# Kernel tuning notes

Measured on AMD Instinct MI355X. Metric: run time of the kernel, lower is better.

The kernel has to match this reference:

```python
import jax, jax.numpy as jnp
import numpy as np

WINDOW_SIZE = 11
CHANNEL = 3
PAD = WINDOW_SIZE // 2
C1 = 0.01 ** 2
C2 = 0.03 ** 2
LEVEL_WEIGHTS = np.array([0.0448, 0.2856, 0.3001, 0.2363, 0.1333], dtype=np.float32)


def _make_window():
    # 1D Gaussian, sigma=1.5, normalized; outer product -> 2D window
    x = np.arange(WINDOW_SIZE, dtype=np.float32)
    g = np.exp(-((x - WINDOW_SIZE // 2) ** 2) / (2.0 * 1.5 ** 2))
    g = g / g.sum()
    w2 = np.outer(g, g).astype(np.float32)  # [11,11]
    # depthwise kernel [C, 1, 11, 11]
    return jnp.asarray(np.tile(w2[None, None], (CHANNEL, 1, 1, 1)))


def setup_inputs() -> dict:
    key = jax.random.key(0)
    k1, k2 = jax.random.split(key)
    img1 = jax.random.uniform(k1, (16, 3, 512, 512), dtype=jnp.float32)
    # correlated second image so cs stays positive (cs**weight well-defined)
    img2 = jnp.clip(img1 + 0.05 * jax.random.normal(k2, img1.shape, dtype=jnp.float32), 0.0, 1.0)
    return {"img1": img1, "img2": img2, "window": _make_window()}


def _dwconv(x, window):
    # depthwise 11x11 conv, SAME padding (pad=5), groups=C
    return jax.lax.conv_general_dilated(
        x, window, window_strides=(1, 1), padding=[(PAD, PAD), (PAD, PAD)],
        feature_group_count=CHANNEL,
        dimension_numbers=("NCHW", "OIHW", "NCHW"))


def _ssim_and_cs(img1, img2, window):
    mu1 = _dwconv(img1, window)
    mu2 = _dwconv(img2, window)
    mu1_sq = mu1 * mu1
    mu2_sq = mu2 * mu2
    mu1_mu2 = mu1 * mu2
    sigma1_sq = _dwconv(img1 * img1, window) - mu1_sq
    sigma2_sq = _dwconv(img2 * img2, window) - mu2_sq
    sigma12 = _dwconv(img1 * img2, window) - mu1_mu2
    cs_map = (2.0 * sigma12 + C2) / (sigma1_sq + sigma2_sq + C2)
    ssim_map = (2.0 * mu1_mu2 + C1) / (mu1_sq + mu2_sq + C1) * cs_map
    return jnp.mean(ssim_map), jnp.mean(cs_map)


def _avg_pool2(x):
    B, C, H, W = x.shape
    return x.reshape(B, C, H // 2, 2, W // 2, 2).mean(axis=(3, 5))


def reference(img1, img2, window):
    weights = jnp.asarray(LEVEL_WEIGHTS)
    levels = weights.shape[0]
    mssim, mcs = [], []
    for i in range(levels):
        s, c = _ssim_and_cs(img1, img2, window)
        mssim.append(s)
        mcs.append(c)
        if i < levels - 1:
            img1 = _avg_pool2(img1)
            img2 = _avg_pool2(img2)
    mssim = jnp.stack(mssim)
    mcs = jnp.stack(mcs)
    return jnp.prod(mcs[:-1] ** weights[:-1]) * mssim[-1] ** weights[-1]
```

## Files before the change

kernel.cpp:

```cpp
#include <hip/hip_runtime.h>
#include <math.h>

#define TW 16
#define SS 58
#define HS 64
#define SC1 0.0001f
#define SC2 0.0009f
#define PLANES 48
#define NSLOT 64

template<int HRt>
struct alignas(16) SmemT {
    float sb[HRt * SS];
    float hb[HRt * HS];
    float rbuf[8];
};

template<int THt>
__device__ __forceinline__ void ssim_tile(
        SmemT<THt + 10>* sm,
        const float* __restrict__ p1, const float* __restrict__ p2,
        int H, int W, int tx, int ty, int level,
        const float* __restrict__ window,
        float* __restrict__ accum,
        float* __restrict__ l1a, float* __restrict__ l1b,
        float* __restrict__ l2a, float* __restrict__ l2b,
        float* __restrict__ l3a, float* __restrict__ l3b,
        float* __restrict__ l4a, float* __restrict__ l4b)
{
    constexpr int HRt = THt + 10;
    const int tid = threadIdx.x;
    float* sb = sm->sb;
    float* hb = sm->hb;

    float g[11];
    {
        float invg5 = 1.0f / sqrtf(window[60]);
        #pragma unroll
        for (int k = 0; k < 11; ++k) g[k] = window[55 + k] * invg5;
    }

    const bool interior = (ty >= 5) && (ty + HRt - 6 < H) &&
                          (tx >= 6) && (tx + 22 <= W);
    if (interior) {
        for (int s = tid; s < HRt * 14; s += 256) {
            int r = s / 14, j = s - r * 14;
            size_t o = (size_t)(ty + r - 5) * W + (tx - 6 + 2 * j);
            float2 v1 = *(const float2*)(p1 + o);
            float2 v2 = *(const float2*)(p2 + o);
            float* d = &sb[SS * r + 4 * j];
            *(float2*)(d)     = make_float2(v1.x + v2.x, v1.x - v2.x);
            *(float2*)(d + 2) = make_float2(v1.y + v2.y, v1.y - v2.y);
        }
    } else {
        for (int s = tid; s < HRt * 14; s += 256) {
            int r = s / 14, j = s - r * 14;
            int gy = ty + r - 5;
            int gx = tx - 6 + 2 * j;
            float2 v1 = make_float2(0.f, 0.f), v2 = make_float2(0.f, 0.f);
            if ((unsigned)gy < (unsigned)H && (unsigned)gx < (unsigned)W) {
                size_t o = (size_t)gy * W + gx;
                v1 = *(const float2*)(p1 + o);
                v2 = *(const float2*)(p2 + o);
            }
            float* d = &sb[SS * r + 4 * j];
            *(float2*)(d)     = make_float2(v1.x + v2.x, v1.x - v2.x);
            *(float2*)(d + 2) = make_float2(v1.y + v2.y, v1.y - v2.y);
        }
    }
    __syncthreads();

    if (l1a) {
        int pc = tid & 7;
        int pr = tid >> 3;
        int r  = 2 * pr + 5;
        int x0 = 2 * (2 * pc + 6);
        const float* a0 = &sb[SS * r + x0];
        float2 p00 = *(const float2*)(a0);
        float2 p01 = *(const float2*)(a0 + 2);
        float2 p10 = *(const float2*)(a0 + SS);
        float2 p11 = *(const float2*)(a0 + SS + 2);
        float su = p00.x + p01.x + p10.x + p11.x;
        float sv = p00.y + p01.y + p10.y + p11.y;
        int W2 = W >> 1;
        size_t o = (size_t)((ty >> 1) + pr) * W2 + (tx >> 1) + pc;
        l1a[o] = 0.125f * (su + sv);
        l1b[o] = 0.125f * (su - sv);
    }

    if (l1a && tid >= 192) {
        const int lane = tid - 192;
        int qr = lane >> 2, qc = lane & 3;
        int rb = 4 * qr + 5, cb = 4 * qc + 6;
        float su = 0.f, sv = 0.f;
        #pragma unroll
        for (int i = 0; i < 4; ++i) {
            int ii = (i + qc) & 3;
            #pragma unroll
            for (int j = 0; j < 4; ++j) {
                int jr = (j + qr) & 3;
                float2 p = *(const float2*)&sb[SS * (rb + ii) + 2 * (cb + jr)];
                su += p.x; sv += p.y;
            }
        }
        float v2a = 0.03125f * (su + sv), v2b = 0.03125f * (su - sv);
        {
            int W4 = W >> 2;
            size_t o = (size_t)((ty >> 2) + qr) * W4 + (tx >> 2) + qc;
            l2a[o] = v2a;
            l2b[o] = v2b;
        }
        float v3a, v3b;
        {
            int tr = (lane >> 1) & 7, tc = lane & 1;
            int l00 = 8 * tr + 2 * tc;
            v3a = 0.25f * (__shfl(v2a, l00) + __shfl(v2a, l00 + 1) +
                           __shfl(v2a, l00 + 4) + __shfl(v2a, l00 + 5));
            v3b = 0.25f * (__shfl(v2b, l00) + __shfl(v2b, l00 + 1) +
                           __shfl(v2b, l00 + 4) + __shfl(v2b, l00 + 5));
            if (lane < 16) {
                int W8 = W >> 3;
                size_t o = (size_t)((ty >> 3) + tr) * W8 + (tx >> 3) + tc;
                l3a[o] = v3a;
                l3b[o] = v3b;
            }
        }
        {
            int ur = lane & 3;
            float v4a = 0.25f * (__shfl(v3a, 4 * ur) + __shfl(v3a, 4 * ur + 1) +
                                 __shfl(v3a, 4 * ur + 2) + __shfl(v3a, 4 * ur + 3));
            float v4b = 0.25f * (__shfl(v3b, 4 * ur) + __shfl(v3b, 4 * ur + 1) +
                                 __shfl(v3b, 4 * ur + 2) + __shfl(v3b, 4 * ur + 3));
            if (lane < 4) {
                int W16 = W >> 4;
                size_t o = (size_t)((ty >> 4) + ur) * W16 + (tx >> 4);
                l4a[o] = v4a;
                l4b[o] = v4b;
            }
        }
    }

    for (int gi = tid; gi < HRt * 8; gi += 256) {
        int r  = gi >> 3;
        int c0 = (gi & 7) << 1;
        const float* src = &sb[SS * r + 2 * (c0 + 1)];
        float mua = 0, mva = 0, qua = 0, qva = 0;
        float mub = 0, mvb = 0, qub = 0, qvb = 0;
        #pragma unroll
        for (int k = 0; k < 12; ++k) {
            float2 uv = *(const float2*)(src + 2 * k);
            float u = uv.x, v = uv.y;
            float u2 = u * u, v2 = v * v;
            if (k < 11) {
                float gk = g[k];
                mua = fmaf(gk, u,  mua);
                mva = fmaf(gk, v,  mva);
                qua = fmaf(gk, u2, qua);
                qva = fmaf(gk, v2, qva);
            }
            if (k >= 1) {
                float gk = g[k - 1];
                mub = fmaf(gk, u,  mub);
                mvb = fmaf(gk, v,  mvb);
                qub = fmaf(gk, u2, qub);
                qvb = fmaf(gk, v2, qvb);
            }
        }
        int rx = (r & 1) << 2;
        *(float4*)&hb[HS * r + ((4 * c0)     ^ rx)] = make_float4(mua, mva, qua, qva);
        *(float4*)&hb[HS * r + ((4 * c0 + 4) ^ rx)] = make_float4(mub, mvb, qub, qvb);
    }
    __syncthreads();

    float ssum = 0.f, csum = 0.f;
    if (tid < 4 * THt) {
        int c  = tid & 15;
        int r0 = (tid >> 4) << 2;
        float MU[4] = {0, 0, 0, 0}, MV[4] = {0, 0, 0, 0};
        float QU[4] = {0, 0, 0, 0}, QV[4] = {0, 0, 0, 0};
        #pragma unroll
        for (int k = 0; k < 14; ++k) {
            int R = r0 + k;
            float4 h = *(const float4*)&hb[HS * R + ((4 * c) ^ ((R & 1) << 2))];
            #pragma unroll
            for (int j = 0; j < 4; ++j) {
                int t = k - j;
                if (t >= 0 && t < 11) {
                    float gk = g[t];
                    MU[j] = fmaf(gk, h.x, MU[j]);
                    MV[j] = fmaf(gk, h.y, MV[j]);
                    QU[j] = fmaf(gk, h.z, QU[j]);
                    QV[j] = fmaf(gk, h.w, QV[j]);
                }
            }
        }
        #pragma unroll
        for (int j = 0; j < 4; ++j) {
            if (ty + r0 + j < H) {
                float P = MU[j] * MU[j], Qm = MV[j] * MV[j];
                float A = 0.5f * (P - Qm);
                float B = 0.5f * (P + Qm);
                float su = 0.5f * (QU[j] + QV[j]);
                float sd = 0.5f * (QU[j] - QV[j]);
                float n1 = A + SC1;
                float d1 = B + SC1;
                float n2 = sd - A + SC2;
                float d2 = su - B + SC2;
                float inv = 1.f / (d1 * d2);
                csum += n2 * d1 * inv;
                ssum += n1 * n2 * inv;
            }
        }
    }

    #pragma unroll
    for (int off = 32; off; off >>= 1) {
        ssum += __shfl_down(ssum, off);
        csum += __shfl_down(csum, off);
    }
    const int wid = tid >> 6, lane = tid & 63;
    if (lane == 0) { sm->rbuf[wid * 2] = ssum; sm->rbuf[wid * 2 + 1] = csum; }
    __syncthreads();
    if (tid == 0) {
        float S = sm->rbuf[0] + sm->rbuf[2] + sm->rbuf[4] + sm->rbuf[6];
        float C = sm->rbuf[1] + sm->rbuf[3] + sm->rbuf[5] + sm->rbuf[7];
        int slot = (blockIdx.x + blockIdx.y * 7 + blockIdx.z * 13) & (NSLOT - 1);
        atomicAdd(&accum[(2 * level) * NSLOT + slot], S);
        atomicAdd(&accum[(2 * level + 1) * NSLOT + slot], C);
    }
}

__global__ __launch_bounds__(256, 4) void ssim_l0(
        const float* __restrict__ img1, const float* __restrict__ img2,
        const float* __restrict__ window, float* __restrict__ accum,
        float* __restrict__ l1a, float* __restrict__ l1b,
        float* __restrict__ l2a, float* __restrict__ l2b,
        float* __restrict__ l3a, float* __restrict__ l3b,
        float* __restrict__ l4a, float* __restrict__ l4b)
{
    __shared__ SmemT<74> sm;
    const int plane = blockIdx.z;
    ssim_tile<64>(&sm,
              img1 + (size_t)plane * 512 * 512,
              img2 + (size_t)plane * 512 * 512,
              512, 512, blockIdx.x * TW, blockIdx.y * 64, 0,
              window, accum,
              l1a + (size_t)plane * 256 * 256, l1b + (size_t)plane * 256 * 256,
              l2a + (size_t)plane * 128 * 128, l2b + (size_t)plane * 128 * 128,
              l3a + (size_t)plane * 64 * 64,   l3b + (size_t)plane * 64 * 64,
              l4a + (size_t)plane * 32 * 32,   l4b + (size_t)plane * 32 * 32);
}

__global__ __launch_bounds__(256, 4) void ssim_rest(
        const float* __restrict__ l1a, const float* __restrict__ l1b,
        const float* __restrict__ l2a, const float* __restrict__ l2b,
        const float* __restrict__ l3a, const float* __restrict__ l3b,
        const float* __restrict__ l4a, const float* __restrict__ l4b,
        const float* __restrict__ window, float* __restrict__ accum)
{
    __shared__ SmemT<74> sm;
    const int x = blockIdx.x;
    const int plane = blockIdx.z;
    int level, H, tix, tiy;
    const float *b1, *b2;
    if (x < 64)      { level = 1; H = 256; tix = x & 15;           tiy = x >> 4;      b1 = l1a; b2 = l1b; }
    else if (x < 80) { level = 2; H = 128; int i = x - 64; tix = i & 7; tiy = i >> 3; b1 = l2a; b2 = l2b; }
    else if (x < 84) { level = 3; H = 64;  int i = x - 80; tix = i;     tiy = 0;      b1 = l3a; b2 = l3b; }
    else             { level = 4; H = 32;  int i = x - 84; tix = i;     tiy = 0;      b1 = l4a; b2 = l4b; }
    const float* p1 = b1 + (size_t)plane * H * H;
    const float* p2 = b2 + (size_t)plane * H * H;
    ssim_tile<64>(&sm, p1, p2, H, H, tix * TW, tiy * 64, level,
              window, accum,
              nullptr, nullptr, nullptr, nullptr,
              nullptr, nullptr, nullptr, nullptr);
}

__global__ void finalize_kernel(const float* __restrict__ accum, float* __restrict__ out) {
    int t = threadIdx.x;
    float sums[10];
    #pragma unroll
    for (int i = 0; i < 10; ++i) {
        float v = accum[i * NSLOT + t];
        #pragma unroll
        for (int off = 32; off; off >>= 1) v += __shfl_down(v, off);
        sums[i] = v;
    }
    if (t == 0) {
        const float w[5] = {0.0448f, 0.2856f, 0.3001f, 0.2363f, 0.1333f};
        float res = 1.f;
        #pragma unroll
        for (int L = 0; L < 4; ++L) {
            float dim = (float)(512 >> L);
            float cnt = (float)PLANES * dim * dim;
            res *= powf(sums[2 * L + 1] / cnt, w[L]);
        }
        float cnt4 = (float)PLANES * 32.f * 32.f;
        res *= powf(sums[8] / cnt4, w[4]);
        out[0] = res;
    }
}

extern "C" void kernel_launch(void* const* d_in, const int* in_sizes, int n_in,
                              void* d_out, int out_size, void* d_ws, size_t ws_size,
                              hipStream_t stream) {
    const float* img1   = (const float*)d_in[0];
    const float* img2   = (const float*)d_in[1];
    const float* window = (const float*)d_in[2];
    float* out = (float*)d_out;
    float* ws  = (float*)d_ws;

    float* accum = ws;
    const size_t S1 = (size_t)PLANES * 256 * 256;
    const size_t S2 = (size_t)PLANES * 128 * 128;
    const size_t S3 = (size_t)PLANES * 64 * 64;
    const size_t S4 = (size_t)PLANES * 32 * 32;
    float* l1a = ws + 1024;    float* l1b = l1a + S1;
    float* l2a = l1b + S1;     float* l2b = l2a + S2;
    float* l3a = l2b + S2;     float* l3b = l3a + S3;
    float* l4a = l3b + S3;     float* l4b = l4a + S4;

    hipMemsetAsync(accum, 0, 10 * NSLOT * sizeof(float), stream);

    ssim_l0<<<dim3(512 / TW, 512 / 64, PLANES), 256, 0, stream>>>(
        img1, img2, window, accum,
        l1a, l1b, l2a, l2b, l3a, l3b, l4a, l4b);

    ssim_rest<<<dim3(86, 1, PLANES), 256, 0, stream>>>(
        l1a, l1b, l2a, l2b, l3a, l3b, l4a, l4b, window, accum);

    finalize_kernel<<<1, 64, 0, stream>>>(accum, out);
}
```

Before: 241.4 us.

## Widen staging halo to 8 for float4 loads and swizzle level-0 block order

```diff
diff --git a/kernel.cpp b/kernel.cpp
--- a/kernel.cpp
+++ b/kernel.cpp
@@ -2,23 +2,23 @@
 #include <math.h>
 
 #define TW 16
-#define SS 58
+#define THT 64
+#define HRT 74
+#define SS 66
 #define HS 64
 #define SC1 0.0001f
 #define SC2 0.0009f
 #define PLANES 48
 #define NSLOT 64
 
-template<int HRt>
-struct alignas(16) SmemT {
-    float sb[HRt * SS];
-    float hb[HRt * HS];
+struct alignas(16) Smem {
+    float sb[HRT * SS];
+    float hb[HRT * HS];
     float rbuf[8];
 };
 
-template<int THt>
 __device__ __forceinline__ void ssim_tile(
-        SmemT<THt + 10>* sm,
+        Smem* sm,
         const float* __restrict__ p1, const float* __restrict__ p2,
         int H, int W, int tx, int ty, int level,
         const float* __restrict__ window,
@@ -28,7 +28,6 @@
         float* __restrict__ l3a, float* __restrict__ l3b,
         float* __restrict__ l4a, float* __restrict__ l4b)
 {
-    constexpr int HRt = THt + 10;
     const int tid = threadIdx.x;
     float* sb = sm->sb;
     float* hb = sm->hb;
@@ -40,23 +39,25 @@
         for (int k = 0; k < 11; ++k) g[k] = window[55 + k] * invg5;
     }
 
-    const bool interior = (ty >= 5) && (ty + HRt - 6 < H) &&
-                          (tx >= 6) && (tx + 22 <= W);
+    const bool interior = (ty >= 5) && (ty + HRT - 6 < H) &&
+                          (tx >= 8) && (tx + 24 <= W);
     if (interior) {
-        for (int s = tid; s < HRt * 14; s += 256) {
-            int r = s / 14, j = s - r * 14;
-            size_t o = (size_t)(ty + r - 5) * W + (tx - 6 + 2 * j);
-            float2 v1 = *(const float2*)(p1 + o);
-            float2 v2 = *(const float2*)(p2 + o);
-            float* d = &sb[SS * r + 4 * j];
-            *(float2*)(d)     = make_float2(v1.x + v2.x, v1.x - v2.x);
-            *(float2*)(d + 2) = make_float2(v1.y + v2.y, v1.y - v2.y);
+        for (int s = tid; s < HRT * 8; s += 256) {
+            int r = s >> 3, j = s & 7;
+            size_t o = (size_t)(ty + r - 5) * W + (tx - 8 + 4 * j);
+            float4 a = *(const float4*)(p1 + o);
+            float4 b = *(const float4*)(p2 + o);
+            float* d = &sb[SS * r + 8 * j];
+            *(float2*)(d)     = make_float2(a.x + b.x, a.x - b.x);
+            *(float2*)(d + 2) = make_float2(a.y + b.y, a.y - b.y);
+            *(float2*)(d + 4) = make_float2(a.z + b.z, a.z - b.z);
+            *(float2*)(d + 6) = make_float2(a.w + b.w, a.w - b.w);
         }
     } else {
-        for (int s = tid; s < HRt * 14; s += 256) {
-            int r = s / 14, j = s - r * 14;
+        for (int s = tid; s < HRT * 16; s += 256) {
+            int r = s >> 4, j = s & 15;
             int gy = ty + r - 5;
-            int gx = tx - 6 + 2 * j;
+            int gx = tx - 8 + 2 * j;
             float2 v1 = make_float2(0.f, 0.f), v2 = make_float2(0.f, 0.f);
             if ((unsigned)gy < (unsigned)H && (unsigned)gx < (unsigned)W) {
                 size_t o = (size_t)gy * W + gx;
@@ -74,7 +75,7 @@
         int pc = tid & 7;
         int pr = tid >> 3;
         int r  = 2 * pr + 5;
-        int x0 = 2 * (2 * pc + 6);
+        int x0 = 2 * (2 * pc + 8);
         const float* a0 = &sb[SS * r + x0];
         float2 p00 = *(const float2*)(a0);
         float2 p01 = *(const float2*)(a0 + 2);
@@ -91,7 +92,7 @@
     if (l1a && tid >= 192) {
         const int lane = tid - 192;
         int qr = lane >> 2, qc = lane & 3;
-        int rb = 4 * qr + 5, cb = 4 * qc + 6;
+        int rb = 4 * qr + 5, cb = 4 * qc + 8;
         float su = 0.f, sv = 0.f;
         #pragma unroll
         for (int i = 0; i < 4; ++i) {
@@ -140,10 +141,10 @@
         }
     }
 
-    for (int gi = tid; gi < HRt * 8; gi += 256) {
+    for (int gi = tid; gi < HRT * 8; gi += 256) {
         int r  = gi >> 3;
         int c0 = (gi & 7) << 1;
-        const float* src = &sb[SS * r + 2 * (c0 + 1)];
+        const float* src = &sb[SS * r + 2 * (c0 + 3)];
         float mua = 0, mva = 0, qua = 0, qva = 0;
         float mub = 0, mvb = 0, qub = 0, qvb = 0;
         #pragma unroll
@@ -173,7 +174,7 @@
     __syncthreads();
 
     float ssum = 0.f, csum = 0.f;
-    if (tid < 4 * THt) {
+    {
         int c  = tid & 15;
         int r0 = (tid >> 4) << 2;
         float MU[4] = {0, 0, 0, 0}, MV[4] = {0, 0, 0, 0};
@@ -238,12 +239,17 @@
         float* __restrict__ l3a, float* __restrict__ l3b,
         float* __restrict__ l4a, float* __restrict__ l4b)
 {
-    __shared__ SmemT<74> sm;
-    const int plane = blockIdx.z;
-    ssim_tile<64>(&sm,
+    __shared__ Smem sm;
+    const int lin = blockIdx.x + (blockIdx.y << 5) + (blockIdx.z << 8);
+    const int swz = (lin & 7) * 1536 + (lin >> 3);
+    const int plane = swz >> 8;
+    const int rem   = swz & 255;
+    const int tyi   = rem >> 5;
+    const int txi   = rem & 31;
+    ssim_tile(&sm,
               img1 + (size_t)plane * 512 * 512,
               img2 + (size_t)plane * 512 * 512,
-              512, 512, blockIdx.x * TW, blockIdx.y * 64, 0,
+              512, 512, txi * TW, tyi * THT, 0,
               window, accum,
               l1a + (size_t)plane * 256 * 256, l1b + (size_t)plane * 256 * 256,
               l2a + (size_t)plane * 128 * 128, l2b + (size_t)plane * 128 * 128,
@@ -258,7 +264,7 @@
         const float* __restrict__ l4a, const float* __restrict__ l4b,
         const float* __restrict__ window, float* __restrict__ accum)
 {
-    __shared__ SmemT<74> sm;
+    __shared__ Smem sm;
     const int x = blockIdx.x;
     const int plane = blockIdx.z;
     int level, H, tix, tiy;
@@ -269,7 +275,7 @@
     else             { level = 4; H = 32;  int i = x - 84; tix = i;     tiy = 0;      b1 = l4a; b2 = l4b; }
     const float* p1 = b1 + (size_t)plane * H * H;
     const float* p2 = b2 + (size_t)plane * H * H;
-    ssim_tile<64>(&sm, p1, p2, H, H, tix * TW, tiy * 64, level,
+    ssim_tile(&sm, p1, p2, H, H, tix * TW, tiy * THT, level,
               window, accum,
               nullptr, nullptr, nullptr, nullptr,
               nullptr, nullptr, nullptr, nullptr);
@@ -321,7 +327,7 @@
 
     hipMemsetAsync(accum, 0, 10 * NSLOT * sizeof(float), stream);
 
-    ssim_l0<<<dim3(512 / TW, 512 / 64, PLANES), 256, 0, stream>>>(
+    ssim_l0<<<dim3(512 / TW, 512 / THT, PLANES), 256, 0, stream>>>(
         img1, img2, window, accum,
         l1a, l1b, l2a, l2b, l3a, l3b, l4a, l4b);
 
```

Result: faster. 222.5 us (-7.8%).
